# Performance work log

Hardware: AMD Instinct MI355X
Metric: run time of the kernel (lower is better)

## Reference

```python
import jax, jax.numpy as jnp
import numpy as np

D_MODEL = 2048
SEQ_LEN = 16   # R is built for context_window=16 in the original module
BATCH = 256


def make_rotary_matrix(m, d):
    # Faithful to get_rotary_matrix: theta = 10000 ** (-2*(i-1)/d)  (note the i-1 bug kept)
    pos = np.arange(m, dtype=np.float64)[:, None]            # [m,1]
    i = np.arange(d // 2, dtype=np.float64)[None, :]         # [1,d/2]
    theta = 10000.0 ** (-2.0 * (i - 1.0) / d)
    ang = pos * theta                                         # [m, d/2]
    cos, sin = np.cos(ang), np.sin(ang)
    R = np.zeros((m, d, d), dtype=np.float32)
    idx = np.arange(d // 2)
    R[:, 2 * idx, 2 * idx] = cos
    R[:, 2 * idx, 2 * idx + 1] = -sin
    R[:, 2 * idx + 1, 2 * idx] = sin
    R[:, 2 * idx + 1, 2 * idx + 1] = cos
    return jnp.asarray(R)


def setup_inputs() -> dict:
    key = jax.random.key(0)
    kx, kq, kk, kv = jax.random.split(key, 4)
    s = 1.0 / np.sqrt(D_MODEL)
    return {
        "x": jax.random.normal(kx, (BATCH, SEQ_LEN, D_MODEL), dtype=jnp.float32),
        "w_q": jax.random.normal(kq, (D_MODEL, D_MODEL), dtype=jnp.float32) * s,
        "w_k": jax.random.normal(kk, (D_MODEL, D_MODEL), dtype=jnp.float32) * s,
        "w_v": jax.random.normal(kv, (D_MODEL, D_MODEL), dtype=jnp.float32) * s,
    }


def reference(x, w_q, w_k, w_v):
    b, m, d = x.shape
    R = make_rotary_matrix(SEQ_LEN, d)[:m]                    # [m,d,d]
    # nn.Linear(bias=False): y = x @ W^T
    q = jnp.einsum("bmd,ed->bme", x, w_q)
    k = jnp.einsum("bmd,ed->bme", x, w_k)
    v = jnp.einsum("bmd,ed->bme", x, w_v)
    # dense per-position rotary rotation via bmm: (q.transpose(0,1) @ R[:m]).transpose(0,1)
    q_rot = jnp.einsum("bmd,mde->bme", q, R)
    k_rot = jnp.einsum("bmd,mde->bme", k, R)
    # scaled_dot_product_attention (dropout treated as eval-mode / disabled)
    scores = jnp.einsum("bme,bne->bmn", q_rot, k_rot) / jnp.sqrt(jnp.float32(d))
    attn = jax.nn.softmax(scores, axis=-1)
    return jnp.einsum("bmn,bne->bme", attn, v)
```

## Files before the change

kernel.cpp:

```cpp
#include <hip/hip_runtime.h>


#define D 2048
#define SEQLEN 16
#define NBATCH 256
#define NROWS (NBATCH * SEQLEN)
#define NX (NROWS * D)
#define NW (D * D)

#define BM 128
#define BN 192
#define BK 64
#define NKT (D / BK)
#define LDSPB ((BM + BN) * BK)

typedef __attribute__((ext_vector_type(8))) short bf16x8;
typedef __attribute__((ext_vector_type(4))) float f32x4;

__device__ __forceinline__ unsigned short f32_to_bf16(float f) {
  unsigned u = __float_as_uint(f);
  unsigned r = 0x7fffu + ((u >> 16) & 1u);
  return (unsigned short)((u + r) >> 16);
}
__device__ __forceinline__ float bf16lo_to_f32(unsigned u) { return __uint_as_float(u << 16); }
__device__ __forceinline__ float bf16hi_to_f32(unsigned u) { return __uint_as_float(u & 0xffff0000u); }

__device__ __forceinline__ bool detect_f32(const ushort* __restrict__ w) {
  int crazy = 0;
#pragma unroll
  for (int i = 0; i < 64; ++i) {
    float v = __uint_as_float((unsigned)w[i] << 16);
    if (!(__builtin_fabsf(v) < 256.0f)) ++crazy;
  }
  return crazy >= 3;
}

__device__ __forceinline__ void glds16(const void* g, void* l) {
  __builtin_amdgcn_global_load_lds(
      (const __attribute__((address_space(1))) void*)g,
      (__attribute__((address_space(3))) void*)l, 16, 0, 0);
}

__global__ __launch_bounds__(256) void convert_inputs(
    const void* __restrict__ x, const void* __restrict__ wq,
    const void* __restrict__ wk, const void* __restrict__ wv,
    ushort* __restrict__ xb, ushort* __restrict__ wqb,
    ushort* __restrict__ wkb, ushort* __restrict__ wvb) {
  if (!detect_f32((const ushort*)wq)) return;
  const float* srcs[4] = {(const float*)x, (const float*)wq, (const float*)wk, (const float*)wv};
  ushort* dsts[4] = {xb, wqb, wkb, wvb};
  const int ns[4] = {NX, NW, NW, NW};
  const int stride = gridDim.x * blockDim.x;
#pragma unroll
  for (int s = 0; s < 4; ++s) {
    const float* __restrict__ src = srcs[s];
    ushort* __restrict__ dst = dsts[s];
    const int n8 = ns[s] / 8;
    for (int i = blockIdx.x * blockDim.x + threadIdx.x; i < n8; i += stride) {
      float4 a = ((const float4*)src)[i * 2];
      float4 b = ((const float4*)src)[i * 2 + 1];
      uint4 o;
      o.x = (unsigned)f32_to_bf16(a.x) | ((unsigned)f32_to_bf16(a.y) << 16);
      o.y = (unsigned)f32_to_bf16(a.z) | ((unsigned)f32_to_bf16(a.w) << 16);
      o.z = (unsigned)f32_to_bf16(b.x) | ((unsigned)f32_to_bf16(b.y) << 16);
      o.w = (unsigned)f32_to_bf16(b.z) | ((unsigned)f32_to_bf16(b.w) << 16);
      ((uint4*)dst)[i] = o;
    }
  }
}

__global__ __launch_bounds__(256, 2) void qkv_rope_gemm(
    const void* __restrict__ Xr, const void* __restrict__ Wqr,
    const void* __restrict__ Wkr, const void* __restrict__ Wvr,
    const ushort* __restrict__ xb, const ushort* __restrict__ wqb,
    const ushort* __restrict__ wkb, const ushort* __restrict__ wvb,
    ushort* __restrict__ Oq, ushort* __restrict__ Ok, ushort* __restrict__ Ov) {
  __shared__ __align__(16) ushort lds[2][LDSPB];

  const bool f32in = detect_f32((const ushort*)Wqr);
  const ushort* __restrict__ X  = f32in ? xb  : (const ushort*)Xr;
  const ushort* __restrict__ Wq = f32in ? wqb : (const ushort*)Wqr;
  const ushort* __restrict__ Wk = f32in ? wkb : (const ushort*)Wkr;
  const ushort* __restrict__ Wv = f32in ? wvb : (const ushort*)Wvr;

  const int m0 = (blockIdx.x >> 5) * BM;
  const int n0 = (blockIdx.x & 31) * BN;

  const int t = threadIdx.x;
  const int wave = t >> 6, lane = t & 63;
  const int quad = lane >> 4, l16 = lane & 15;
  const int wr = wave >> 1, wc = wave & 1;

  const int srow = t >> 3;
  const int scol = ((t & 7) ^ (srow & 7)) * 8;
  const ushort* gA = X + (size_t)(m0 + srow) * D + scol;
  const ushort* gB[6];
#pragma unroll
  for (int c = 0; c < 6; ++c) {
    const int ng = n0 + c * 32 + srow;
    const int z = ng >> 11;
    gB[c] = ((z == 0) ? Wq : (z == 1) ? Wk : Wv) + (size_t)(ng & 2047) * D + scol;
  }

  f32x4 acc[4][6] = {};

  auto STAGE = [&](int b, int kt) {
    const int kc = kt * BK;
#pragma unroll
    for (int c = 0; c < 4; ++c)
      glds16(gA + (size_t)c * 32 * D + kc, &lds[b][c * 2048 + t * 8]);
#pragma unroll
    for (int c = 0; c < 6; ++c)
      glds16(gB[c] + kc, &lds[b][BM * BK + c * 2048 + t * 8]);
  };

  STAGE(0, 0);
  STAGE(1, 1);

  const int swz = (l16 & 7) << 3;

  for (int kt = 0; kt < NKT; ++kt) {
    const int cur = kt & 1;

    if (kt < NKT - 1) asm volatile("s_waitcnt vmcnt(10)" ::: "memory");
    else              asm volatile("s_waitcnt vmcnt(0)"  ::: "memory");
    __builtin_amdgcn_s_barrier();
    __builtin_amdgcn_sched_barrier(0);

    const ushort* Ab = &lds[cur][0];
    const ushort* Bb = &lds[cur][BM * BK];

    bf16x8 af2[2][4], bfr2[2][6];
#pragma unroll
    for (int ks = 0; ks < 2; ++ks) {
      const int ko = (ks * 32 + quad * 8) ^ swz;
#pragma unroll
      for (int f = 0; f < 4; ++f)
        af2[ks][f] = *(const bf16x8*)(Ab + (wr * 64 + f * 16 + l16) * 64 + ko);
#pragma unroll
      for (int g = 0; g < 6; ++g)
        bfr2[ks][g] = *(const bf16x8*)(Bb + (wc * 96 + g * 16 + l16) * 64 + ko);
    }
    asm volatile("s_waitcnt lgkmcnt(0)" ::: "memory");
    __builtin_amdgcn_s_barrier();
    if (kt + 2 < NKT) STAGE(cur, kt + 2);
    __builtin_amdgcn_sched_barrier(0);

    __builtin_amdgcn_s_setprio(1);
#pragma unroll
    for (int ks = 0; ks < 2; ++ks)
#pragma unroll
      for (int f = 0; f < 4; ++f)
#pragma unroll
        for (int g = 0; g < 6; ++g)
          acc[f][g] = __builtin_amdgcn_mfma_f32_16x16x32_bf16(
              af2[ks][f], bfr2[ks][g], acc[f][g], 0, 0, 0);
    __builtin_amdgcn_s_setprio(0);
  }

#pragma unroll
  for (int g = 0; g < 6; ++g) {
    const int eg = n0 + wc * 96 + g * 16 + l16;
    const int z = eg >> 11;
    const int e = eg & 2047;
    const bool rope = (z != 2);
    ushort* __restrict__ O = (z == 0) ? Oq : (z == 1) ? Ok : Ov;
    float cs[4] = {}, sn[4] = {};
    if (rope) {
      const float theta = exp2f(-0.012976281620653759f * ((float)(e >> 1) - 1.0f));
#pragma unroll
      for (int r = 0; r < 4; ++r)
        __sincosf((float)(quad * 4 + r) * theta, &sn[r], &cs[r]);
    }
#pragma unroll
    for (int f = 0; f < 4; ++f) {
      const size_t rbase = (size_t)(m0 + wr * 64 + f * 16 + quad * 4) * D;
#pragma unroll
      for (int r = 0; r < 4; ++r) {
        float v = acc[f][g][r];
        float p = __shfl_xor(v, 1);
        float o = v;
        if (rope)
          o = (e & 1) ? (v * cs[r] - p * sn[r])
                      : (v * cs[r] + p * sn[r]);
        O[rbase + (size_t)r * D + e] = f32_to_bf16(o);
      }
    }
  }
}

__global__ __launch_bounds__(512) void rope_attention(
    const ushort* __restrict__ Q, const ushort* __restrict__ K,
    const ushort* __restrict__ V, const void* __restrict__ Wqr, void* __restrict__ OutRaw) {
  __shared__ float sc[8][16][16];
  __shared__ float at[16][16];
  const bool f32out = detect_f32((const ushort*)Wqr);
  const int b = blockIdx.x;
  const int t = threadIdx.x;
  const int wave = t >> 6, lane = t & 63;
  const int quad = lane >> 4, l16 = lane & 15;

  const ushort* Qb = Q + (size_t)b * (SEQLEN * D);
  const ushort* Kb = K + (size_t)b * (SEQLEN * D);

  f32x4 acc = {0.f, 0.f, 0.f, 0.f};
  const ushort* qp = Qb + l16 * D + wave * 256 + quad * 8;
  const ushort* kp = Kb + l16 * D + wave * 256 + quad * 8;
#pragma unroll
  for (int s = 0; s < 8; ++s) {
    bf16x8 a = *(const bf16x8*)(qp + s * 32);
    bf16x8 bb = *(const bf16x8*)(kp + s * 32);
    acc = __builtin_amdgcn_mfma_f32_16x16x32_bf16(a, bb, acc, 0, 0, 0);
  }
#pragma unroll
  for (int r = 0; r < 4; ++r)
    sc[wave][quad * 4 + r][l16] = acc[r];
  __syncthreads();

  if (t < 256) {
    const int m = t >> 4, n = t & 15;
    float s = (sc[0][m][n] + sc[1][m][n] + sc[2][m][n] + sc[3][m][n] +
               sc[4][m][n] + sc[5][m][n] + sc[6][m][n] + sc[7][m][n]) * 0.02209708691207961f;
    float mx = s;
#pragma unroll
    for (int off = 8; off; off >>= 1) mx = fmaxf(mx, __shfl_xor(mx, off, 16));
    float e = __expf(s - mx);
    float sum = e;
#pragma unroll
    for (int off = 8; off; off >>= 1) sum += __shfl_xor(sum, off, 16);
    at[m][n] = e / sum;
  }
  __syncthreads();

  const ushort* Vb = V + (size_t)b * (SEQLEN * D);
  const int e0 = t * 4;
  uint2 vr[16];
#pragma unroll
  for (int n = 0; n < 16; ++n)
    vr[n] = *(const uint2*)(Vb + n * D + e0);

  for (int m = 0; m < 16; ++m) {
    float av[4] = {0.f, 0.f, 0.f, 0.f};
#pragma unroll
    for (int n = 0; n < 16; ++n) {
      const float a = at[m][n];
      const uint2 u = vr[n];
      av[0] = fmaf(a, bf16lo_to_f32(u.x), av[0]);
      av[1] = fmaf(a, bf16hi_to_f32(u.x), av[1]);
      av[2] = fmaf(a, bf16lo_to_f32(u.y), av[2]);
      av[3] = fmaf(a, bf16hi_to_f32(u.y), av[3]);
    }
    if (f32out) {
      float* Ob = (float*)OutRaw + (size_t)b * (SEQLEN * D) + m * D + e0;
      float4 o0 = {av[0], av[1], av[2], av[3]};
      *(float4*)Ob = o0;
    } else {
      uint2 o;
      o.x = (unsigned)f32_to_bf16(av[0]) | ((unsigned)f32_to_bf16(av[1]) << 16);
      o.y = (unsigned)f32_to_bf16(av[2]) | ((unsigned)f32_to_bf16(av[3]) << 16);
      *(uint2*)((ushort*)OutRaw + (size_t)b * (SEQLEN * D) + m * D + e0) = o;
    }
  }
}

extern "C" void kernel_launch(void* const* d_in, const int* in_sizes, int n_in,
                              void* d_out, int out_size, void* d_ws, size_t ws_size,
                              hipStream_t stream) {
  const void* x  = d_in[0];
  const void* wq = d_in[1];
  const void* wk = d_in[2];
  const void* wv = d_in[3];
  ushort* ws = (ushort*)d_ws;
  ushort* xb  = ws;
  ushort* wqb = ws + NX;
  ushort* wkb = ws + NX + NW;
  ushort* wvb = ws + NX + 2 * (size_t)NW;
  ushort* q = ws + NX + 3 * (size_t)NW;
  ushort* k = q + NX;
  ushort* v = k + NX;

  convert_inputs<<<1536, 256, 0, stream>>>(x, wq, wk, wv, xb, wqb, wkb, wvb);
  qkv_rope_gemm<<<dim3(1024), 256, 0, stream>>>(x, wq, wk, wv, xb, wqb, wkb, wvb, q, k, v);
  rope_attention<<<NBATCH, 512, 0, stream>>>(q, k, v, wq, (ushort*)d_out);
}
```

Measured before the change: 240.1 us.

## Fuse QK^T partial scores into QKV GEMM epilogue, drop Q/K global writes

Each GEMM block now owns a 64-column slice of Q, K and V for the same feature range. After rotary it stages Q and K in shared memory and computes partial 16x16 attention scores per batch, writing fp32 partials to a scratch buffer instead of storing full Q and K to global memory. The attention kernel sums the 32 partials, applies softmax, and does the AV product with wider 8-element vectors over 256 threads. This removes the Q/K round trip through global memory, at the cost of an extra epilogue phase, a barrier and a partial-score buffer.

```diff
diff --git a/kernel.cpp b/kernel.cpp
--- a/kernel.cpp
+++ b/kernel.cpp
@@ -74,7 +74,7 @@
     const void* __restrict__ Wkr, const void* __restrict__ Wvr,
     const ushort* __restrict__ xb, const ushort* __restrict__ wqb,
     const ushort* __restrict__ wkb, const ushort* __restrict__ wvb,
-    ushort* __restrict__ Oq, ushort* __restrict__ Ok, ushort* __restrict__ Ov) {
+    ushort* __restrict__ Ov, float* __restrict__ Sp) {
   __shared__ __align__(16) ushort lds[2][LDSPB];
 
   const bool f32in = detect_f32((const ushort*)Wqr);
@@ -84,7 +84,8 @@
   const ushort* __restrict__ Wv = f32in ? wvb : (const ushort*)Wvr;
 
   const int m0 = (blockIdx.x >> 5) * BM;
-  const int n0 = (blockIdx.x & 31) * BN;
+  const int eb = blockIdx.x & 31;
+  const int e0 = eb * 64;
 
   const int t = threadIdx.x;
   const int wave = t >> 6, lane = t & 63;
@@ -97,9 +98,8 @@
   const ushort* gB[6];
 #pragma unroll
   for (int c = 0; c < 6; ++c) {
-    const int ng = n0 + c * 32 + srow;
-    const int z = ng >> 11;
-    gB[c] = ((z == 0) ? Wq : (z == 1) ? Wk : Wv) + (size_t)(ng & 2047) * D + scol;
+    const ushort* Wz = (c < 2) ? Wq : (c < 4) ? Wk : Wv;
+    gB[c] = Wz + (size_t)(e0 + (c & 1) * 32 + srow) * D + scol;
   }
 
   f32x4 acc[4][6] = {};
@@ -158,69 +158,79 @@
     __builtin_amdgcn_s_setprio(0);
   }
 
+  ushort* qk_lds = &lds[0][0];
 #pragma unroll
   for (int g = 0; g < 6; ++g) {
-    const int eg = n0 + wc * 96 + g * 16 + l16;
-    const int z = eg >> 11;
-    const int e = eg & 2047;
-    const bool rope = (z != 2);
-    ushort* __restrict__ O = (z == 0) ? Oq : (z == 1) ? Ok : Ov;
-    float cs[4] = {}, sn[4] = {};
-    if (rope) {
-      const float theta = exp2f(-0.012976281620653759f * ((float)(e >> 1) - 1.0f));
+    const int ncol = wc * 96 + g * 16;
+    const int z = ncol >> 6;
+    const int el = (ncol & 63) + l16;
+    const int eg = e0 + el;
+    if (z < 2) {
+      const float theta = exp2f(-0.012976281620653759f * ((float)(eg >> 1) - 1.0f));
+      float cs[4], sn[4];
 #pragma unroll
       for (int r = 0; r < 4; ++r)
         __sincosf((float)(quad * 4 + r) * theta, &sn[r], &cs[r]);
-    }
-#pragma unroll
-    for (int f = 0; f < 4; ++f) {
-      const size_t rbase = (size_t)(m0 + wr * 64 + f * 16 + quad * 4) * D;
-#pragma unroll
-      for (int r = 0; r < 4; ++r) {
-        float v = acc[f][g][r];
-        float p = __shfl_xor(v, 1);
-        float o = v;
-        if (rope)
-          o = (e & 1) ? (v * cs[r] - p * sn[r])
-                      : (v * cs[r] + p * sn[r]);
-        O[rbase + (size_t)r * D + e] = f32_to_bf16(o);
+#pragma unroll
+      for (int f = 0; f < 4; ++f) {
+#pragma unroll
+        for (int r = 0; r < 4; ++r) {
+          float v = acc[f][g][r];
+          float p = __shfl_xor(v, 1);
+          float o = (eg & 1) ? (v * cs[r] - p * sn[r])
+                             : (v * cs[r] + p * sn[r]);
+          const int row = wr * 64 + f * 16 + quad * 4 + r;
+          const int colw = el ^ ((row & 7) << 3);
+          qk_lds[z * 8192 + row * 64 + colw] = f32_to_bf16(o);
+        }
       }
-    }
-  }
-}
-
-__global__ __launch_bounds__(512) void rope_attention(
-    const ushort* __restrict__ Q, const ushort* __restrict__ K,
-    const ushort* __restrict__ V, const void* __restrict__ Wqr, void* __restrict__ OutRaw) {
-  __shared__ float sc[8][16][16];
+    } else {
+#pragma unroll
+      for (int f = 0; f < 4; ++f) {
+        const size_t rbase = (size_t)(m0 + wr * 64 + f * 16 + quad * 4) * D;
+#pragma unroll
+        for (int r = 0; r < 4; ++r)
+          Ov[rbase + (size_t)r * D + eg] = f32_to_bf16(acc[f][g][r]);
+      }
+    }
+  }
+  __syncthreads();
+
+  const int gb0 = (m0 >> 4);
+#pragma unroll
+  for (int bb = 0; bb < 2; ++bb) {
+    const int bi = wave * 2 + bb;
+    const int row = bi * 16 + l16;
+    f32x4 s = {0.f, 0.f, 0.f, 0.f};
+#pragma unroll
+    for (int ks = 0; ks < 2; ++ks) {
+      const int ko = (ks * 32 + quad * 8) ^ swz;
+      bf16x8 aq = *(const bf16x8*)(qk_lds + row * 64 + ko);
+      bf16x8 bk = *(const bf16x8*)(qk_lds + 8192 + row * 64 + ko);
+      s = __builtin_amdgcn_mfma_f32_16x16x32_bf16(aq, bk, s, 0, 0, 0);
+    }
+    float* sp = Sp + ((size_t)(eb * NBATCH + gb0 + bi) << 8);
+#pragma unroll
+    for (int r = 0; r < 4; ++r)
+      sp[(quad * 4 + r) * 16 + l16] = s[r];
+  }
+}
+
+__global__ __launch_bounds__(256) void rope_attention(
+    const float* __restrict__ Sp, const ushort* __restrict__ V,
+    const void* __restrict__ Wqr, void* __restrict__ OutRaw) {
   __shared__ float at[16][16];
   const bool f32out = detect_f32((const ushort*)Wqr);
   const int b = blockIdx.x;
   const int t = threadIdx.x;
-  const int wave = t >> 6, lane = t & 63;
-  const int quad = lane >> 4, l16 = lane & 15;
-
-  const ushort* Qb = Q + (size_t)b * (SEQLEN * D);
-  const ushort* Kb = K + (size_t)b * (SEQLEN * D);
-
-  f32x4 acc = {0.f, 0.f, 0.f, 0.f};
-  const ushort* qp = Qb + l16 * D + wave * 256 + quad * 8;
-  const ushort* kp = Kb + l16 * D + wave * 256 + quad * 8;
-#pragma unroll
-  for (int s = 0; s < 8; ++s) {
-    bf16x8 a = *(const bf16x8*)(qp + s * 32);
-    bf16x8 bb = *(const bf16x8*)(kp + s * 32);
-    acc = __builtin_amdgcn_mfma_f32_16x16x32_bf16(a, bb, acc, 0, 0, 0);
-  }
-#pragma unroll
-  for (int r = 0; r < 4; ++r)
-    sc[wave][quad * 4 + r][l16] = acc[r];
-  __syncthreads();
-
-  if (t < 256) {
+
+  {
     const int m = t >> 4, n = t & 15;
-    float s = (sc[0][m][n] + sc[1][m][n] + sc[2][m][n] + sc[3][m][n] +
-               sc[4][m][n] + sc[5][m][n] + sc[6][m][n] + sc[7][m][n]) * 0.02209708691207961f;
+    float s = 0.f;
+#pragma unroll
+    for (int ebi = 0; ebi < 32; ++ebi)
+      s += Sp[((size_t)(ebi * NBATCH + b) << 8) + t];
+    s *= 0.02209708691207961f;
     float mx = s;
 #pragma unroll
     for (int off = 8; off; off >>= 1) mx = fmaxf(mx, __shfl_xor(mx, off, 16));
@@ -233,32 +243,40 @@
   __syncthreads();
 
   const ushort* Vb = V + (size_t)b * (SEQLEN * D);
-  const int e0 = t * 4;
-  uint2 vr[16];
+  const int e0 = t * 8;
+  uint4 vr[16];
 #pragma unroll
   for (int n = 0; n < 16; ++n)
-    vr[n] = *(const uint2*)(Vb + n * D + e0);
+    vr[n] = *(const uint4*)(Vb + n * D + e0);
 
   for (int m = 0; m < 16; ++m) {
-    float av[4] = {0.f, 0.f, 0.f, 0.f};
+    float av[8] = {0.f, 0.f, 0.f, 0.f, 0.f, 0.f, 0.f, 0.f};
 #pragma unroll
     for (int n = 0; n < 16; ++n) {
       const float a = at[m][n];
-      const uint2 u = vr[n];
+      const uint4 u = vr[n];
       av[0] = fmaf(a, bf16lo_to_f32(u.x), av[0]);
       av[1] = fmaf(a, bf16hi_to_f32(u.x), av[1]);
       av[2] = fmaf(a, bf16lo_to_f32(u.y), av[2]);
       av[3] = fmaf(a, bf16hi_to_f32(u.y), av[3]);
+      av[4] = fmaf(a, bf16lo_to_f32(u.z), av[4]);
+      av[5] = fmaf(a, bf16hi_to_f32(u.z), av[5]);
+      av[6] = fmaf(a, bf16lo_to_f32(u.w), av[6]);
+      av[7] = fmaf(a, bf16hi_to_f32(u.w), av[7]);
     }
     if (f32out) {
       float* Ob = (float*)OutRaw + (size_t)b * (SEQLEN * D) + m * D + e0;
       float4 o0 = {av[0], av[1], av[2], av[3]};
-      *(float4*)Ob = o0;
+      float4 o1 = {av[4], av[5], av[6], av[7]};
+      ((float4*)Ob)[0] = o0;
+      ((float4*)Ob)[1] = o1;
     } else {
-      uint2 o;
+      uint4 o;
       o.x = (unsigned)f32_to_bf16(av[0]) | ((unsigned)f32_to_bf16(av[1]) << 16);
       o.y = (unsigned)f32_to_bf16(av[2]) | ((unsigned)f32_to_bf16(av[3]) << 16);
-      *(uint2*)((ushort*)OutRaw + (size_t)b * (SEQLEN * D) + m * D + e0) = o;
+      o.z = (unsigned)f32_to_bf16(av[4]) | ((unsigned)f32_to_bf16(av[5]) << 16);
+      o.w = (unsigned)f32_to_bf16(av[6]) | ((unsigned)f32_to_bf16(av[7]) << 16);
+      *(uint4*)((ushort*)OutRaw + (size_t)b * (SEQLEN * D) + m * D + e0) = o;
     }
   }
 }
@@ -275,11 +293,10 @@
   ushort* wqb = ws + NX;
   ushort* wkb = ws + NX + NW;
   ushort* wvb = ws + NX + 2 * (size_t)NW;
-  ushort* q = ws + NX + 3 * (size_t)NW;
-  ushort* k = q + NX;
-  ushort* v = k + NX;
+  ushort* v   = ws + NX + 3 * (size_t)NW;
+  float*  Sp  = (float*)(ws + 2 * (size_t)NX + 3 * (size_t)NW);
 
   convert_inputs<<<1536, 256, 0, stream>>>(x, wq, wk, wv, xb, wqb, wkb, wvb);
-  qkv_rope_gemm<<<dim3(1024), 256, 0, stream>>>(x, wq, wk, wv, xb, wqb, wkb, wvb, q, k, v);
-  rope_attention<<<NBATCH, 512, 0, stream>>>(q, k, v, wq, (ushort*)d_out);
-}
+  qkv_rope_gemm<<<dim3(1024), 256, 0, stream>>>(x, wq, wk, wv, xb, wqb, wkb, wvb, v, Sp);
+  rope_attention<<<NBATCH, 256, 0, stream>>>(Sp, v, wq, (ushort*)d_out);
+}
```

Result: faster. 228.9 us, median of 3 (-4.7%).
